# Kernel tuning notes

Measured on AMD Instinct MI355X. Metric: run time of the kernel, lower is better.

The kernel has to match this reference:

```python
import jax, jax.numpy as jnp
import numpy as np
import itertools


def _dwconv(x, w, b, pad, dil):
    # depthwise conv3d, x: [B,C,H,W,D], w: [C,1,k,k,k]
    out = jax.lax.conv_general_dilated(
        x, w, (1, 1, 1), [(pad, pad)] * 3, rhs_dilation=(dil, dil, dil),
        dimension_numbers=('NCDHW', 'OIDHW', 'NCDHW'), feature_group_count=x.shape[1])
    return out + b[None, :, None, None, None]


def _conv(x, w, b, pad):
    out = jax.lax.conv_general_dilated(
        x, w, (1, 1, 1), [(pad, pad)] * 3,
        dimension_numbers=('NCDHW', 'OIDHW', 'NCDHW'))
    return out + b[None, :, None, None, None]


def _pw(x, w, b):
    # 1x1x1 conv: x [B,C,H,W,D], w [O,C]
    return jnp.einsum('bchwd,oc->bohwd', x, w) + b[None, :, None, None, None]


def _deform_conv3d(x, off_w, off_b, w, b):
    # DeformConvPack-style: offsets from a regular 3x3x3 conv, then
    # trilinearly-interpolated gather at (base + kernel tap + offset), then GEMM.
    B, C, H, W, D = x.shape
    K = 27
    dt = x.dtype
    off = _conv(x, off_w, off_b, 1).reshape(B, K, 3, H, W, D)  # per-tap (dh,dw,dd)
    gh = jnp.arange(H, dtype=dt)
    gw = jnp.arange(W, dtype=dt)
    gd = jnp.arange(D, dtype=dt)
    base = jnp.stack(jnp.meshgrid(gh, gw, gd, indexing='ij'), 0)  # [3,H,W,D]
    t = jnp.arange(-1, 2, dtype=dt)  # kernel taps, padding=1
    taps = jnp.stack(jnp.meshgrid(t, t, t, indexing='ij'), -1).reshape(K, 3)
    pos = base[None] + taps[:, :, None, None, None]  # [K,3,H,W,D]
    pos = pos[None] + off  # [B,K,3,H,W,D]
    i0 = jnp.floor(pos)
    frac = pos - i0  # [B,K,3,H,W,D]
    i0 = i0.astype(jnp.int32)
    N = H * W * D
    xf = x.reshape(B, C, N)
    hi = jnp.array([H - 1, W - 1, D - 1], jnp.int32)[None, None, :, None, None, None]
    acc = jnp.zeros((B, C, K * N), dt)
    for corner in itertools.product((0, 1), repeat=3):
        c = jnp.array(corner, jnp.int32)[None, None, :, None, None, None]
        idx = i0 + c
        wgt = jnp.prod(jnp.where(c == 1, frac, 1.0 - frac), axis=2)  # [B,K,H,W,D]
        valid = jnp.all((idx >= 0) & (idx <= hi), axis=2)
        ic = jnp.clip(idx, 0, hi)
        flat = (ic[:, :, 0] * W + ic[:, :, 1]) * D + ic[:, :, 2]  # [B,K,H,W,D]
        g = jnp.take_along_axis(xf, flat.reshape(B, 1, K * N), axis=2)  # [B,C,K*N]
        acc = acc + g * (wgt * valid.astype(dt)).reshape(B, 1, K * N)
    sampled = acc.reshape(B, C, K, N)
    out = jnp.einsum('bckn,ock->bon', sampled, w.reshape(w.shape[0], C, K))
    out = out + b[None, :, None]
    return out.reshape(B, -1, H, W, D)


def _forward(x, proj1_w, proj1_b, conv0_w, conv0_b, convsp_w, convsp_b,
             off_w, off_b, dcn_w, dcn_b, conv1_w, conv1_b, proj2_w, proj2_b,
             B, C, H, W, D):
    xv = jnp.transpose(x, (0, 2, 1)).reshape(B, C, H, W, D)
    shortcut = xv
    h = jax.nn.gelu(_pw(xv, proj1_w, proj1_b), approximate=False)
    u = h
    a = _dwconv(h, conv0_w, conv0_b, 2, 1)        # 5x5x5 depthwise
    a = _dwconv(a, convsp_w, convsp_b, 9, 3)      # 7x7x7 depthwise, dilation 3
    a = _deform_conv3d(a, off_w, off_b, dcn_w, dcn_b)
    a = _pw(a, conv1_w, conv1_b)
    h = u * a
    h = _pw(h, proj2_w, proj2_b)
    out = h + shortcut
    return jnp.transpose(out.reshape(B, C, H * W * D), (0, 2, 1))


def setup_inputs() -> dict:
    key = jax.random.key(0)
    ks = jax.random.split(key, 8)
    B, C, H, W, D = 1, 64, 32, 32, 32
    N = H * W * D
    r = lambda k, s, sc: jax.random.normal(k, s, jnp.float32) * np.float32(sc)
    inv = lambda f: 1.0 / np.sqrt(f)
    return {
        'x': jax.random.normal(ks[0], (B, N, C), jnp.float32),
        'proj1_w': r(ks[1], (C, C), inv(C)), 'proj1_b': jnp.zeros((C,), jnp.float32),
        'conv0_w': r(ks[2], (C, 1, 5, 5, 5), inv(125)), 'conv0_b': jnp.zeros((C,), jnp.float32),
        'convsp_w': r(ks[3], (C, 1, 7, 7, 7), inv(343)), 'convsp_b': jnp.zeros((C,), jnp.float32),
        'off_w': r(ks[4], (81, C, 3, 3, 3), 0.01 * inv(27 * C)), 'off_b': jnp.zeros((81,), jnp.float32),
        'dcn_w': r(ks[5], (C, C, 3, 3, 3), inv(27 * C)), 'dcn_b': jnp.zeros((C,), jnp.float32),
        'conv1_w': r(ks[6], (C, C), inv(C)), 'conv1_b': jnp.zeros((C,), jnp.float32),
        'proj2_w': r(ks[7], (C, C), inv(C)), 'proj2_b': jnp.zeros((C,), jnp.float32),
        'B': B, 'C': C, 'H': H, 'W': W, 'D': D,
    }


def reference(x, proj1_w, proj1_b, conv0_w, conv0_b, convsp_w, convsp_b,
              off_w, off_b, dcn_w, dcn_b, conv1_w, conv1_b, proj2_w, proj2_b,
              B, C, H, W, D):
    return _forward(x, proj1_w, proj1_b, conv0_w, conv0_b, convsp_w, convsp_b,
                    off_w, off_b, dcn_w, dcn_b, conv1_w, conv1_b, proj2_w, proj2_b,
                    B, C, H, W, D)
```

## Files before the change

### kernel.cpp

```cpp
#include <hip/hip_runtime.h>
#include <math.h>

#define NSP 32768
#define NCH 64

typedef _Float16 half8 __attribute__((ext_vector_type(8)));
typedef _Float16 half4 __attribute__((ext_vector_type(4)));
typedef _Float16 half2v __attribute__((ext_vector_type(2)));
typedef float f32x4 __attribute__((ext_vector_type(4)));

__global__ __launch_bounds__(256) void k_proj1m(const float* __restrict__ x,
        const half8* __restrict__ Wp1, const float* __restrict__ b,
        _Float16* __restrict__ Uh) {
    __shared__ __align__(16) _Float16 Sx[64 * 72];
    int t = threadIdx.x;
    int n0 = blockIdx.x * 64;
    int lane = t & 63, wv = t >> 6;
    for (int i = wv; i < 64; i += 4) {
        float v = x[(size_t)(n0 + i) * 64 + lane];
        Sx[i * 72 + lane] = (_Float16)v;
    }
    __syncthreads();
    int pl = lane & 15, g = lane >> 4;
    int ob = wv;
    const half8* wbase = Wp1 + ob * 64 + lane;
    #pragma unroll
    for (int nt = 0; nt < 4; ++nt) {
        f32x4 acc4 = {0.f, 0.f, 0.f, 0.f};
        const _Float16* sb = &Sx[(nt * 16 + pl) * 72 + g * 8];
        #pragma unroll
        for (int kb = 0; kb < 2; ++kb) {
            half8 af = wbase[kb * 256];
            half8 bf = *(const half8*)(sb + kb * 32);
            acc4 = __builtin_amdgcn_mfma_f32_16x16x32_f16(af, bf, acc4, 0, 0, 0);
        }
        int n = n0 + nt * 16 + pl;
        #pragma unroll
        for (int r = 0; r < 4; ++r) {
            int o = ob * 16 + g * 4 + r;
            float a = acc4[r] + b[o];
            float gv = 0.5f * a * (1.0f + erff(a * 0.70710678118654752f));
            Uh[(size_t)o * NSP + n] = (_Float16)gv;
        }
    }
}

__global__ __launch_bounds__(256) void k_dw5(const _Float16* __restrict__ in,
        const float* __restrict__ w, const float* __restrict__ b,
        _Float16* __restrict__ out) {
    __shared__ float Sb5[2][20 * 38];
    int t = threadIdx.x;
    int bid = blockIdx.x;
    int blk = (bid & 7) * 128 + (bid >> 3);
    int c  = blk >> 4;
    int hq = (blk >> 1) & 7;
    int wq = blk & 1;
    int d  = t & 31;
    int wbloc = t >> 5;
    int wb = wq * 8 + wbloc;
    const float* wc = w + c * 125;
    const _Float16* src = in + ((size_t)c << 15);

    for (int idx = t; idx < 160; idx += 256) {
        int bi = idx / 80, r = idx % 80;
        int wi = r >> 2, e = r & 3;
        int Dp = (e < 2) ? e : 32 + e;
        Sb5[bi][wi * 38 + Dp] = 0.f;
    }

    float bc = b[c];
    float acc[4][2];
    #pragma unroll
    for (int a = 0; a < 4; ++a) { acc[a][0] = bc; acc[a][1] = bc; }

    #define STAGE5(m)                                                        \
        { int hh_ = 4 * hq + (m) - 2;                                        \
          if ((unsigned)hh_ < 32u) {                                         \
            const _Float16* row_ = src + (hh_ << 10);                        \
            for (int idx = t; idx < 80; idx += 256) {                        \
                int wi = idx >> 2, oct = idx & 3;                            \
                int wj = 16 * wq - 2 + wi;                                   \
                half8 vv = (half8)(_Float16)0.f;                             \
                if ((unsigned)wj < 32u)                                      \
                    vv = *(const half8*)&row_[(wj << 5) + oct * 8];          \
                float* dst = &Sb5[(m) & 1][wi * 38 + 2 + oct * 8];           \
                dst[0] = (float)vv[0]; dst[1] = (float)vv[1];                \
                dst[2] = (float)vv[2]; dst[3] = (float)vv[3];                \
                dst[4] = (float)vv[4]; dst[5] = (float)vv[5];                \
                dst[6] = (float)vv[6]; dst[7] = (float)vv[7];                \
            } } }

    STAGE5(0)
    __syncthreads();
    #pragma unroll 1
    for (int m = 0; m < 8; ++m) {
        if (m < 7) STAGE5(m + 1)
        int hh = 4 * hq + m - 2;
        if ((unsigned)hh < 32u) {
            float v[6][5];
            const float* sb = &Sb5[m & 1][0];
            #pragma unroll
            for (int jc = 0; jc < 6; ++jc)
                #pragma unroll
                for (int l = 0; l < 5; ++l)
                    v[jc][l] = sb[(2 * wbloc + jc) * 38 + d + l];
            #pragma unroll
            for (int a = 0; a < 4; ++a) {
                if (a <= m && m <= a + 4) {
                    const float* wr = wc + (m - a) * 25;
                    float s0 = 0.f, s1 = 0.f;
                    #pragma unroll
                    for (int j = 0; j < 5; ++j)
                        #pragma unroll
                        for (int l = 0; l < 5; ++l) {
                            float wv2 = wr[j * 5 + l];
                            s0 += wv2 * v[j][l];
                            s1 += wv2 * v[j + 1][l];
                        }
                    acc[a][0] += s0;
                    acc[a][1] += s1;
                }
            }
        }
        __syncthreads();
    }
    #pragma unroll
    for (int a = 0; a < 4; ++a)
        #pragma unroll
        for (int bb = 0; bb < 2; ++bb)
            out[(size_t)c * NSP + ((4 * hq + a) << 10) + ((2 * wb + bb) << 5) + d]
                = (_Float16)acc[a][bb];
    #undef STAGE5
}

__global__ __launch_bounds__(256) void k_dw7(const _Float16* __restrict__ in,
        const float* __restrict__ w, const float* __restrict__ b,
        _Float16* __restrict__ out) {
    __shared__ float Sb7[2][26 * 52];
    int t = threadIdx.x;
    int bid = blockIdx.x;
    int blk = (bid & 7) * 96 + (bid >> 3);
    int c  = blk / 12;
    int h0 = (blk % 12) >> 2;
    int wq = blk & 3;
    int d  = t & 31;
    int wloc = t >> 5;
    int w_ = wq * 8 + wloc;
    const float* wc = w + c * 343;
    const _Float16* src = in + ((size_t)c << 15);

    for (int idx = t; idx < 936; idx += 256) {
        int bi = idx / 468, r = idx % 468;
        int wi = r / 18, e = r % 18;
        int Dp = (e < 9) ? e : 32 + e;
        Sb7[bi][wi * 52 + Dp] = 0.f;
    }

    float bc = b[c];
    float acc[11];
    #pragma unroll
    for (int a = 0; a < 11; ++a) acc[a] = bc;

    #define STAGE7(m)                                                        \
        { int hh_ = h0 + 3 * (m) - 9;                                        \
          if ((unsigned)hh_ < 32u) {                                         \
            const _Float16* row_ = src + (hh_ << 10);                        \
            for (int idx = t; idx < 104; idx += 256) {                       \
                int wi = idx >> 2, oct = idx & 3;                            \
                int wj = 8 * wq - 9 + wi;                                    \
                half8 vv = (half8)(_Float16)0.f;                             \
                if ((unsigned)wj < 32u)                                      \
                    vv = *(const half8*)&row_[(wj << 5) + oct * 8];          \
                float* dst = &Sb7[(m) & 1][wi * 52 + 9 + oct * 8];           \
                dst[0] = (float)vv[0]; dst[1] = (float)vv[1];                \
                dst[2] = (float)vv[2]; dst[3] = (float)vv[3];                \
                dst[4] = (float)vv[4]; dst[5] = (float)vv[5];                \
                dst[6] = (float)vv[6]; dst[7] = (float)vv[7];                \
            } } }

    STAGE7(0)
    __syncthreads();
    #pragma unroll 1
    for (int m = 0; m < 17; ++m) {
        if (m < 16) STAGE7(m + 1)
        int hh = h0 + 3 * m - 9;
        if ((unsigned)hh < 32u) {
            float vf[49];
            const float* sb = &Sb7[m & 1][0];
            #pragma unroll
            for (int jw = 0; jw < 7; ++jw)
                #pragma unroll
                for (int l = 0; l < 7; ++l)
                    vf[jw * 7 + l] = sb[(wloc + 3 * jw) * 52 + d + 3 * l];
            #pragma unroll
            for (int a = 0; a < 11; ++a) {
                if (a <= m && m <= a + 6) {
                    const float* wr = wc + (m - a) * 49;
                    float sA = 0.f, sB = 0.f;
                    #pragma unroll
                    for (int q = 0; q < 24; ++q) {
                        sA = fmaf(wr[2 * q],     vf[2 * q],     sA);
                        sB = fmaf(wr[2 * q + 1], vf[2 * q + 1], sB);
                    }
                    acc[a] += sA + sB + wr[48] * vf[48];
                }
            }
        }
        __syncthreads();
    }
    #pragma unroll
    for (int a = 0; a < 11; ++a) {
        int h = h0 + 3 * a;
        if (h < 32)
            out[(size_t)c * NSP + (h << 10) + (w_ << 5) + d] = (_Float16)acc[a];
    }
    #undef STAGE7
}

__global__ __launch_bounds__(256) void k_tr(const _Float16* __restrict__ in,
        _Float16* __restrict__ outh) {
    __shared__ __align__(16) _Float16 tile[64 * 74];
    int t = threadIdx.x;
    int n0 = blockIdx.x * 64;
    #pragma unroll
    for (int i = 0; i < 2; ++i) {
        int u = i * 256 + t;
        int c = u >> 3, oct = u & 7;
        half8 v = *(const half8*)&in[(size_t)c * NSP + n0 + oct * 8];
        *(half8*)&tile[c * 74 + oct * 8] = v;
    }
    __syncthreads();
    #pragma unroll
    for (int i = 0; i < 2; ++i) {
        int u = i * 256 + t;
        int nl = u >> 3, co = u & 7;
        half8 r;
        #pragma unroll
        for (int j = 0; j < 8; ++j) r[j] = tile[(co * 8 + j) * 74 + nl];
        *(half8*)&outh[(size_t)(n0 + nl) * 64 + co * 8] = r;
    }
}

__global__ __launch_bounds__(256) void k_wpack(const float* __restrict__ dw,
        _Float16* __restrict__ Wp) {
    int idx = blockIdx.x * 256 + threadIdx.x;
    int j = idx & 7;
    int l = (idx >> 3) & 63;
    int obk = idx >> 9;
    int ob = obk & 3, kb = obk >> 2;
    int o = ob * 16 + (l & 15);
    int Kp = kb * 32 + (l >> 4) * 8 + j;
    int k = Kp >> 6, c = Kp & 63;
    Wp[idx] = (_Float16)dw[(size_t)o * 1728 + c * 27 + k];
}

__global__ __launch_bounds__(256) void k_wpack_off(const float* __restrict__ ow,
        _Float16* __restrict__ Wp2) {
    int idx = blockIdx.x * 256 + threadIdx.x;
    int j = idx & 7;
    int l = (idx >> 3) & 63;
    int obk = idx >> 9;
    int ob = obk % 6, kb = obk / 6;
    int o = ob * 16 + (l & 15);
    int Kp = kb * 32 + (l >> 4) * 8 + j;
    int k = Kp >> 6, c = Kp & 63;
    Wp2[idx] = (o < 81) ? (_Float16)ow[(size_t)o * 1728 + c * 27 + k]
                        : (_Float16)0.f;
}

__global__ __launch_bounds__(256) void k_wpack64(const float* __restrict__ w,
        _Float16* __restrict__ Wp) {
    int idx = blockIdx.x * 256 + threadIdx.x;
    int j = idx & 7;
    int l = (idx >> 3) & 63;
    int obk = idx >> 9;
    int ob = obk & 3, kb = obk >> 2;
    int o = ob * 16 + (l & 15);
    int Kp = kb * 32 + (l >> 4) * 8 + j;
    Wp[idx] = (_Float16)w[o * 64 + Kp];
}

__global__ __launch_bounds__(384) void k_offg(const _Float16* __restrict__ aTh,
        const half8* __restrict__ Wp2, const float* __restrict__ obias,
        float* __restrict__ off) {
    __shared__ __align__(16) _Float16 S2[2][4 * 34 * 72];
    int t = threadIdx.x;
    int bid = blockIdx.x;
    int blk = (bid & 7) * 64 + (bid >> 3);
    int h = blk >> 4, w0 = (blk & 15) * 2;
    int n0 = (h << 10) + (w0 << 5);
    int lane = t & 63, wv = t >> 6;
    int co8 = (lane & 7) << 3;

    for (int u = t; u < 1152; u += 384) {
        int bi = u / 576, r2 = u % 576;
        int nbw = r2 / 144, r3 = r2 % 144;
        int dd = (r3 >= 72) ? 33 : 0, cc = r3 % 72;
        S2[bi][(nbw * 34 + dd) * 72 + cc] = (_Float16)0.f;
    }

    int pl = lane & 15, g = lane >> 4;
    int obi = wv;
    f32x4 acc[4];
    #pragma unroll
    for (int i = 0; i < 4; ++i) acc[i] = (f32x4){0.f, 0.f, 0.f, 0.f};
    const half8* wb = Wp2 + obi * 64 + lane;

    #define OSTAGE(kh)                                                        \
        { int hh_ = h + (kh) - 1;                                            \
          bool okh_ = (unsigned)hh_ < 32u;                                   \
          for (int u = wv; u < 16; u += 6) {                                 \
              int nbw = u >> 2, oct = u & 3;                                 \
              int wj = w0 + nbw - 1;                                         \
              int di = oct * 8 + (lane >> 3);                                \
              bool ok = okh_ & ((unsigned)wj < 32u);                         \
              half8 vv = (half8)(_Float16)0.f;                               \
              if (ok) vv = *(const half8*)(aTh +                             \
                  ((size_t)((((hh_ << 5) + wj) << 5) + di)) * 64 + co8);     \
              *(half8*)&S2[(kh) & 1][(nbw * 34 + 1 + di) * 72 + co8] = vv;   \
          } }

    #define OCOMP(kh)                                                        \
        { const _Float16* sb = &S2[(kh) & 1][pl * 72 + g * 8];               \
          _Pragma("unroll")                                                  \
          for (int kk = 0; kk < 18; ++kk) {                                  \
              int kglob = (kh) * 9 + (kk >> 1);                              \
              int kw3 = (kglob / 3) % 3, kd = kglob % 3;                     \
              half8 af = wb[(size_t)((kh) * 18 + kk) * 384];                 \
              _Pragma("unroll")                                              \
              for (int pt = 0; pt < 4; ++pt) {                               \
                  int row = ((pt >> 1) + kw3) * 34 + (pt & 1) * 16 + kd;     \
                  half8 bf = *(const half8*)(sb + row * 72 + (kk & 1) * 32); \
                  acc[pt] = __builtin_amdgcn_mfma_f32_16x16x32_f16(          \
                                af, bf, acc[pt], 0, 0, 0);                   \
              }                                                              \
          } }

    OSTAGE(0)
    __syncthreads();
    OSTAGE(1)
    OCOMP(0)
    __syncthreads();
    OSTAGE(2)
    OCOMP(1)
    __syncthreads();
    OCOMP(2)
    #undef OSTAGE
    #undef OCOMP

    #pragma unroll
    for (int pt = 0; pt < 4; ++pt) {
        #pragma unroll
        for (int r = 0; r < 4; ++r) {
            int o = obi * 16 + g * 4 + r;
            if (o < 81)
                off[(size_t)o * NSP + n0 + pt * 16 + pl] = acc[pt][r] + obias[o];
        }
    }
}

__global__ __launch_bounds__(256) void k_deform(const _Float16* __restrict__ aTh,
        const float* __restrict__ off, const half8* __restrict__ Wp,
        const float* __restrict__ db, _Float16* __restrict__ dcnT) {
    __shared__ __align__(16) _Float16 S[32 * 456];
    __shared__ __align__(16) _Float16 TPF[864 * 4];
    __shared__ int TPv[864];
    int t = threadIdx.x;
    int bid = blockIdx.x;
    int blk = (bid & 7) * 128 + (bid >> 3);
    int n0 = blk * 32;
    int lane = t & 63, wv = t >> 6;

    for (int idx = t; idx < 864; idx += 256) {
        int p = idx & 31, k = idx >> 5;
        int n = n0 + p;
        int h = n >> 10, w = (n >> 5) & 31, d = n & 31;
        float ph = (float)(h + k / 9 - 1)       + off[(size_t)(k * 3 + 0) * NSP + n];
        float pw = (float)(w + (k / 3) % 3 - 1) + off[(size_t)(k * 3 + 1) * NSP + n];
        float pd = (float)(d + k % 3 - 1)       + off[(size_t)(k * 3 + 2) * NSP + n];
        float fh = floorf(ph), fw = floorf(pw), fd = floorf(pd);
        int ih = (int)fh, iw = (int)fw, id = (int)fd;
        int nb0 = ih * 1024 + iw * 32 + id;
        int mask = 0;
        #pragma unroll
        for (int cb = 0; cb < 8; ++cb) {
            int hh = ih + ((cb >> 2) & 1);
            int wq = iw + ((cb >> 1) & 1);
            int dq = id + (cb & 1);
            bool ok = ((unsigned)hh < 32u) & ((unsigned)wq < 32u) & ((unsigned)dq < 32u);
            mask |= (ok ? 1 : 0) << cb;
        }
        TPv[idx] = ((nb0 + 4096) << 8) | mask;
        half4 f;
        f[0] = (_Float16)(ph - fh);
        f[1] = (_Float16)(pw - fw);
        f[2] = (_Float16)(pd - fd);
        f[3] = (_Float16)0.f;
        *(half4*)&TPF[idx * 4] = f;
    }
    __syncthreads();

    int p8 = lane >> 3, co = lane & 7;
    int pl = lane & 15, g = lane >> 4;
    f32x4 acc[2];
    acc[0] = (f32x4){0.f, 0.f, 0.f, 0.f};
    acc[1] = (f32x4){0.f, 0.f, 0.f, 0.f};
    const half8* wbase = Wp + wv * 64 + lane;
    const _Float16* sbase0 = &S[pl * 456 + g * 8];
    const _Float16* sbase1 = &S[(16 + pl) * 456 + g * 8];

    #define DCHUNK(T0, NT)                                                   \
        for (int u = wv; u < (NT) * 4; u += 4) {                             \
            int kk = u >> 2, pg = u & 3;                                     \
            int p = pg * 8 + p8;                                             \
            int tap = ((T0) + kk) * 32 + p;                                  \
            int v = TPv[tap];                                                \
            int nb = (v >> 8) - 4096, mask = v & 255;                        \
            half4 f = *(const half4*)&TPF[tap * 4];                          \
            _Float16 one = (_Float16)1.f;                                    \
            _Float16 rh = f[0], rw = f[1], rd = f[2];                        \
            _Float16 h0 = one - rh, w0 = one - rw, d0 = one - rd;            \
            _Float16 t00 = h0 * w0, t01 = h0 * rw;                           \
            _Float16 t10 = rh * w0, t11 = rh * rw;                           \
            half2v a0 = (half2v)0, a1 = (half2v)0, a2 = (half2v)0,           \
                   a3 = (half2v)0;                                           \
            _Pragma("unroll")                                                \
            for (int i = 0; i < 8; ++i) {                                    \
                int nn = nb + ((i >> 2) & 1) * 1024 + ((i >> 1) & 1) * 32    \
                       + (i & 1);                                            \
                bool okc = (mask >> i) & 1;                                  \
                size_t ad = okc ? ((size_t)nn << 6) : 0;                     \
                half8 vv = *(const half8*)(aTh + ad + (co << 3));            \
                _Float16 txy = (i & 4) ? ((i & 2) ? t11 : t10)               \
                                       : ((i & 2) ? t01 : t00);              \
                _Float16 wg = txy * ((i & 1) ? rd : d0);                     \
                wg = okc ? wg : (_Float16)0.f;                               \
                half2v wg2 = {wg, wg};                                       \
                a0 += (half2v){vv[0], vv[1]} * wg2;                          \
                a1 += (half2v){vv[2], vv[3]} * wg2;                          \
                a2 += (half2v){vv[4], vv[5]} * wg2;                          \
                a3 += (half2v){vv[6], vv[7]} * wg2;                          \
            }                                                                \
            half8 r;                                                         \
            r[0] = a0[0]; r[1] = a0[1]; r[2] = a1[0]; r[3] = a1[1];          \
            r[4] = a2[0]; r[5] = a2[1]; r[6] = a3[0]; r[7] = a3[1];          \
            *(half8*)&S[p * 456 + kk * 64 + (co << 3)] = r;                  \
        }                                                                    \
        __syncthreads();                                                     \
        _Pragma("unroll")                                                    \
        for (int kb = 0; kb < (NT) * 2; ++kb) {                              \
            half8 af = wbase[(size_t)(2 * (T0) + kb) * 256];                 \
            half8 bf0 = *(const half8*)(sbase0 + kb * 32);                   \
            half8 bf1 = *(const half8*)(sbase1 + kb * 32);                   \
            acc[0] = __builtin_amdgcn_mfma_f32_16x16x32_f16(af, bf0,         \
                         acc[0], 0, 0, 0);                                   \
            acc[1] = __builtin_amdgcn_mfma_f32_16x16x32_f16(af, bf1,         \
                         acc[1], 0, 0, 0);                                   \
        }                                                                    \
        __syncthreads();

    DCHUNK(0, 7)
    DCHUNK(7, 7)
    DCHUNK(14, 7)
    DCHUNK(21, 6)
    #undef DCHUNK

    #pragma unroll
    for (int pt = 0; pt < 2; ++pt) {
        half4 hv;
        #pragma unroll
        for (int r2 = 0; r2 < 4; ++r2) {
            int o = wv * 16 + g * 4 + r2;
            hv[r2] = (_Float16)(acc[pt][r2] + db[o]);
        }
        *(half4*)&dcnT[(size_t)(n0 + pt * 16 + pl) * 64 + wv * 16 + g * 4] = hv;
    }
}

__global__ __launch_bounds__(256) void k_finalm(const _Float16* __restrict__ dcnT,
        const _Float16* __restrict__ Uh, const float* __restrict__ x,
        const half8* __restrict__ Wc1, const float* __restrict__ c1b,
        const half8* __restrict__ Wp2f, const float* __restrict__ p2b,
        float* __restrict__ out) {
    __shared__ __align__(16) _Float16 Sd[64 * 72];
    __shared__ __align__(16) _Float16 Sh[64 * 72];
    int t = threadIdx.x;
    int n0 = blockIdx.x * 64;
    int lane = t & 63, wv = t >> 6;
    #pragma unroll
    for (int i = 0; i < 2; ++i) {
        int u = i * 256 + t;
        int nl = u >> 3, oct = u & 7;
        *(half8*)&Sd[nl * 72 + oct * 8] =
            *(const half8*)&dcnT[(size_t)(n0 + nl) * 64 + oct * 8];
    }
    __syncthreads();

    int pl = lane & 15, g = lane >> 4;
    int ob = wv;
    const half8* w1 = Wc1 + ob * 64 + lane;
    #pragma unroll
    for (int nt = 0; nt < 4; ++nt) {
        f32x4 acc4 = {0.f, 0.f, 0.f, 0.f};
        const _Float16* sb = &Sd[(nt * 16 + pl) * 72 + g * 8];
        #pragma unroll
        for (int kb = 0; kb < 2; ++kb) {
            half8 af = w1[kb * 256];
            half8 bf = *(const half8*)(sb + kb * 32);
            acc4 = __builtin_amdgcn_mfma_f32_16x16x32_f16(af, bf, acc4, 0, 0, 0);
        }
        int n = n0 + nt * 16 + pl;
        int o0 = ob * 16 + g * 4;
        float4 bb = *(const float4*)&c1b[o0];
        half4 hv;
        hv[0] = (_Float16)((float)Uh[(size_t)(o0 + 0) * NSP + n] * (acc4[0] + bb.x));
        hv[1] = (_Float16)((float)Uh[(size_t)(o0 + 1) * NSP + n] * (acc4[1] + bb.y));
        hv[2] = (_Float16)((float)Uh[(size_t)(o0 + 2) * NSP + n] * (acc4[2] + bb.z));
        hv[3] = (_Float16)((float)Uh[(size_t)(o0 + 3) * NSP + n] * (acc4[3] + bb.w));
        *(half4*)&Sh[(nt * 16 + pl) * 72 + o0] = hv;
    }
    __syncthreads();

    const half8* w2 = Wp2f + ob * 64 + lane;
    #pragma unroll
    for (int nt = 0; nt < 4; ++nt) {
        f32x4 acc4 = {0.f, 0.f, 0.f, 0.f};
        const _Float16* sb = &Sh[(nt * 16 + pl) * 72 + g * 8];
        #pragma unroll
        for (int kb = 0; kb < 2; ++kb) {
            half8 af = w2[kb * 256];
            half8 bf = *(const half8*)(sb + kb * 32);
            acc4 = __builtin_amdgcn_mfma_f32_16x16x32_f16(af, bf, acc4, 0, 0, 0);
        }
        int n = n0 + nt * 16 + pl;
        int o0 = ob * 16 + g * 4;
        float4 bb = *(const float4*)&p2b[o0];
        float4 xr = *(const float4*)&x[(size_t)n * 64 + o0];
        float4 ov;
        ov.x = acc4[0] + bb.x + xr.x;
        ov.y = acc4[1] + bb.y + xr.y;
        ov.z = acc4[2] + bb.z + xr.z;
        ov.w = acc4[3] + bb.w + xr.w;
        *(float4*)&out[(size_t)n * 64 + o0] = ov;
    }
}

extern "C" void kernel_launch(void* const* d_in, const int* in_sizes, int n_in,
                              void* d_out, int out_size, void* d_ws, size_t ws_size,
                              hipStream_t stream) {
    const float* x   = (const float*)d_in[0];
    const float* p1w = (const float*)d_in[1];
    const float* p1b = (const float*)d_in[2];
    const float* c0w = (const float*)d_in[3];
    const float* c0b = (const float*)d_in[4];
    const float* csw = (const float*)d_in[5];
    const float* csb = (const float*)d_in[6];
    const float* ofw = (const float*)d_in[7];
    const float* ofb = (const float*)d_in[8];
    const float* dcw = (const float*)d_in[9];
    const float* dcb = (const float*)d_in[10];
    const float* c1w = (const float*)d_in[11];
    const float* c1b = (const float*)d_in[12];
    const float* p2w = (const float*)d_in[13];
    const float* p2b = (const float*)d_in[14];
    float* out = (float*)d_out;

    char* ws = (char*)d_ws;
    const size_t CN2 = (size_t)NCH * NSP * 2;
    _Float16* Uh   = (_Float16*)(ws);
    _Float16* T0h  = (_Float16*)(ws + CN2);
    _Float16* T1h  = (_Float16*)(ws + 2 * CN2);
    _Float16* aTh  = (_Float16*)(ws + 3 * CN2);
    float*    OFFp = (float*)(ws + 4 * CN2);
    _Float16* dcnT = (_Float16*)(ws + 4 * CN2 + (size_t)81 * NSP * 4);
    _Float16* Wp   = dcnT + (size_t)NSP * 64;
    _Float16* Wp2  = Wp + 110592;
    _Float16* Wp1  = Wp2 + 165888;
    _Float16* Wc1  = Wp1 + 4096;
    _Float16* Wp2f = Wc1 + 4096;

    k_wpack64  <<<16, 256, 0, stream>>>(p1w, Wp1);
    k_wpack64  <<<16, 256, 0, stream>>>(c1w, Wc1);
    k_wpack64  <<<16, 256, 0, stream>>>(p2w, Wp2f);
    k_wpack    <<<432, 256, 0, stream>>>(dcw, Wp);
    k_wpack_off<<<648, 256, 0, stream>>>(ofw, Wp2);
    k_proj1m   <<<NSP / 64, 256, 0, stream>>>(x, (const half8*)Wp1, p1b, Uh);
    k_dw5      <<<1024, 256, 0, stream>>>(Uh, c0w, c0b, T0h);
    k_dw7      <<<768, 256, 0, stream>>>(T0h, csw, csb, T1h);
    k_tr       <<<NSP / 64, 256, 0, stream>>>(T1h, aTh);
    k_offg     <<<512, 384, 0, stream>>>(aTh, (const half8*)Wp2, ofb, OFFp);
    k_deform   <<<1024, 256, 0, stream>>>(aTh, OFFp, (const half8*)Wp, dcb, dcnT);
    k_finalm   <<<NSP / 64, 256, 0, stream>>>(dcnT, Uh, x, (const half8*)Wc1, c1b,
                                              (const half8*)Wp2f, p2b, out);
}
```

Before: 125.5 us.

## Store offsets point-major, halve offg tile, merge weight-pack kernels

The offset conv output moves from channel-major [81][N] to point-major [N][27x4], with each tap padded to a float4. This lets the deform kernel fetch each tap's (dh,dw,dd) with one vector load instead of three strided loads. The offset GEMM kernel now handles one w-column (32 points) per block with twice as many blocks, and transposes results through LDS for coalesced float4 stores. The five weight-packing launches are merged into one kernel. The costs are a larger offset buffer (108 vs 81 floats per point), an extra LDS pass with syncs, and less weight reuse per offg block.

Measured after the change: 120.8 us. 3.7% less time.

```diff
diff --git a/kernel.cpp b/kernel.cpp
--- a/kernel.cpp
+++ b/kernel.cpp
@@ -241,95 +241,104 @@
     }
 }
 
-__global__ __launch_bounds__(256) void k_wpack(const float* __restrict__ dw,
-        _Float16* __restrict__ Wp) {
-    int idx = blockIdx.x * 256 + threadIdx.x;
-    int j = idx & 7;
-    int l = (idx >> 3) & 63;
-    int obk = idx >> 9;
-    int ob = obk & 3, kb = obk >> 2;
-    int o = ob * 16 + (l & 15);
-    int Kp = kb * 32 + (l >> 4) * 8 + j;
-    int k = Kp >> 6, c = Kp & 63;
-    Wp[idx] = (_Float16)dw[(size_t)o * 1728 + c * 27 + k];
-}
-
-__global__ __launch_bounds__(256) void k_wpack_off(const float* __restrict__ ow,
+__global__ __launch_bounds__(256) void k_wpack_all(
+        const float* __restrict__ p1w, const float* __restrict__ c1w,
+        const float* __restrict__ p2w, const float* __restrict__ dcw,
+        const float* __restrict__ ofw,
+        _Float16* __restrict__ Wp1, _Float16* __restrict__ Wc1,
+        _Float16* __restrict__ Wp2f, _Float16* __restrict__ Wp,
         _Float16* __restrict__ Wp2) {
-    int idx = blockIdx.x * 256 + threadIdx.x;
-    int j = idx & 7;
-    int l = (idx >> 3) & 63;
-    int obk = idx >> 9;
-    int ob = obk % 6, kb = obk / 6;
-    int o = ob * 16 + (l & 15);
-    int Kp = kb * 32 + (l >> 4) * 8 + j;
-    int k = Kp >> 6, c = Kp & 63;
-    Wp2[idx] = (o < 81) ? (_Float16)ow[(size_t)o * 1728 + c * 27 + k]
-                        : (_Float16)0.f;
-}
-
-__global__ __launch_bounds__(256) void k_wpack64(const float* __restrict__ w,
-        _Float16* __restrict__ Wp) {
-    int idx = blockIdx.x * 256 + threadIdx.x;
-    int j = idx & 7;
-    int l = (idx >> 3) & 63;
-    int obk = idx >> 9;
-    int ob = obk & 3, kb = obk >> 2;
-    int o = ob * 16 + (l & 15);
-    int Kp = kb * 32 + (l >> 4) * 8 + j;
-    Wp[idx] = (_Float16)w[o * 64 + Kp];
+    int bidx = blockIdx.x;
+    int t = threadIdx.x;
+    if (bidx < 48) {
+        const float* w = (bidx < 16) ? p1w : (bidx < 32) ? c1w : p2w;
+        _Float16* Wd   = (bidx < 16) ? Wp1 : (bidx < 32) ? Wc1 : Wp2f;
+        int idx = (bidx & 15) * 256 + t;
+        int j = idx & 7;
+        int l = (idx >> 3) & 63;
+        int obk = idx >> 9;
+        int ob = obk & 3, kb = obk >> 2;
+        int o = ob * 16 + (l & 15);
+        int Kp = kb * 32 + (l >> 4) * 8 + j;
+        Wd[idx] = (_Float16)w[o * 64 + Kp];
+    } else if (bidx < 480) {
+        int idx = (bidx - 48) * 256 + t;
+        int j = idx & 7;
+        int l = (idx >> 3) & 63;
+        int obk = idx >> 9;
+        int ob = obk & 3, kb = obk >> 2;
+        int o = ob * 16 + (l & 15);
+        int Kp = kb * 32 + (l >> 4) * 8 + j;
+        int k = Kp >> 6, c = Kp & 63;
+        Wp[idx] = (_Float16)dcw[(size_t)o * 1728 + c * 27 + k];
+    } else {
+        int idx = (bidx - 480) * 256 + t;
+        int j = idx & 7;
+        int l = (idx >> 3) & 63;
+        int obk = idx >> 9;
+        int ob = obk % 6, kb = obk / 6;
+        int o = ob * 16 + (l & 15);
+        int Kp = kb * 32 + (l >> 4) * 8 + j;
+        int k = Kp >> 6, c = Kp & 63;
+        Wp2[idx] = (o < 81) ? (_Float16)ofw[(size_t)o * 1728 + c * 27 + k]
+                            : (_Float16)0.f;
+    }
 }
 
 __global__ __launch_bounds__(384) void k_offg(const _Float16* __restrict__ aTh,
         const half8* __restrict__ Wp2, const float* __restrict__ obias,
-        float* __restrict__ off) {
-    __shared__ __align__(16) _Float16 S2[2][4 * 34 * 72];
+        float* __restrict__ OFFn) {
+    __shared__ __align__(16) char SMEM[29376];
+    _Float16* S2 = (_Float16*)SMEM;
+    float*    TF = (float*)SMEM;
+    const int SB = 3 * 34 * 72;
     int t = threadIdx.x;
     int bid = blockIdx.x;
-    int blk = (bid & 7) * 64 + (bid >> 3);
-    int h = blk >> 4, w0 = (blk & 15) * 2;
-    int n0 = (h << 10) + (w0 << 5);
+    int blk = (bid & 7) * 128 + (bid >> 3);
+    int h = blk >> 5, w = blk & 31;
+    int n0 = blk << 5;
     int lane = t & 63, wv = t >> 6;
     int co8 = (lane & 7) << 3;
 
-    for (int u = t; u < 1152; u += 384) {
-        int bi = u / 576, r2 = u % 576;
+    for (int u = t; u < 864; u += 384) {
+        int bi = u / 432, r2 = u % 432;
         int nbw = r2 / 144, r3 = r2 % 144;
         int dd = (r3 >= 72) ? 33 : 0, cc = r3 % 72;
-        S2[bi][(nbw * 34 + dd) * 72 + cc] = (_Float16)0.f;
+        S2[bi * SB + (nbw * 34 + dd) * 72 + cc] = (_Float16)0.f;
     }
 
     int pl = lane & 15, g = lane >> 4;
     int obi = wv;
-    f32x4 acc[4];
-    #pragma unroll
-    for (int i = 0; i < 4; ++i) acc[i] = (f32x4){0.f, 0.f, 0.f, 0.f};
+    f32x4 acc[2];
+    acc[0] = (f32x4){0.f, 0.f, 0.f, 0.f};
+    acc[1] = (f32x4){0.f, 0.f, 0.f, 0.f};
     const half8* wb = Wp2 + obi * 64 + lane;
 
     #define OSTAGE(kh)                                                        \
         { int hh_ = h + (kh) - 1;                                            \
           bool okh_ = (unsigned)hh_ < 32u;                                   \
-          for (int u = wv; u < 16; u += 6) {                                 \
+          for (int u = wv; u < 12; u += 6) {                                 \
               int nbw = u >> 2, oct = u & 3;                                 \
-              int wj = w0 + nbw - 1;                                         \
+              int wj = w + nbw - 1;                                          \
               int di = oct * 8 + (lane >> 3);                                \
               bool ok = okh_ & ((unsigned)wj < 32u);                         \
               half8 vv = (half8)(_Float16)0.f;                               \
               if (ok) vv = *(const half8*)(aTh +                             \
                   ((size_t)((((hh_ << 5) + wj) << 5) + di)) * 64 + co8);     \
-              *(half8*)&S2[(kh) & 1][(nbw * 34 + 1 + di) * 72 + co8] = vv;   \
+              *(half8*)&S2[((kh) & 1) * SB + (nbw * 34 + 1 + di) * 72 + co8] \
+                  = vv;                                                      \
           } }
 
     #define OCOMP(kh)                                                        \
-        { const _Float16* sb = &S2[(kh) & 1][pl * 72 + g * 8];               \
+        { const _Float16* sb = &S2[((kh) & 1) * SB + pl * 72 + g * 8];       \
           _Pragma("unroll")                                                  \
           for (int kk = 0; kk < 18; ++kk) {                                  \
               int kglob = (kh) * 9 + (kk >> 1);                              \
               int kw3 = (kglob / 3) % 3, kd = kglob % 3;                     \
               half8 af = wb[(size_t)((kh) * 18 + kk) * 384];                 \
               _Pragma("unroll")                                              \
-              for (int pt = 0; pt < 4; ++pt) {                               \
-                  int row = ((pt >> 1) + kw3) * 34 + (pt & 1) * 16 + kd;     \
+              for (int pt = 0; pt < 2; ++pt) {                               \
+                  int row = kw3 * 34 + pt * 16 + kd;                         \
                   half8 bf = *(const half8*)(sb + row * 72 + (kk & 1) * 32); \
                   acc[pt] = __builtin_amdgcn_mfma_f32_16x16x32_f16(          \
                                 af, bf, acc[pt], 0, 0, 0);                   \
@@ -348,19 +357,29 @@
     #undef OSTAGE
     #undef OCOMP
 
-    #pragma unroll
-    for (int pt = 0; pt < 4; ++pt) {
+    __syncthreads();
+    #pragma unroll
+    for (int pt = 0; pt < 2; ++pt) {
+        int pos = pt * 16 + pl;
         #pragma unroll
         for (int r = 0; r < 4; ++r) {
             int o = obi * 16 + g * 4 + r;
-            if (o < 81)
-                off[(size_t)o * NSP + n0 + pt * 16 + pl] = acc[pt][r] + obias[o];
-        }
+            if (o < 81) {
+                int slot = (o / 3) * 4 + o % 3;
+                TF[pos * 108 + slot] = acc[pt][r] + obias[o];
+            }
+        }
+    }
+    __syncthreads();
+    for (int u = t; u < 864; u += 384) {
+        int row = u / 27, q = u - row * 27;
+        float4 v = *(const float4*)&TF[row * 108 + q * 4];
+        *(float4*)&OFFn[(size_t)(n0 + row) * 108 + q * 4] = v;
     }
 }
 
 __global__ __launch_bounds__(256) void k_deform(const _Float16* __restrict__ aTh,
-        const float* __restrict__ off, const half8* __restrict__ Wp,
+        const float* __restrict__ OFFn, const half8* __restrict__ Wp,
         const float* __restrict__ db, _Float16* __restrict__ dcnT) {
     __shared__ __align__(16) _Float16 S[32 * 456];
     __shared__ __align__(16) _Float16 TPF[864 * 4];
@@ -375,9 +394,10 @@
         int p = idx & 31, k = idx >> 5;
         int n = n0 + p;
         int h = n >> 10, w = (n >> 5) & 31, d = n & 31;
-        float ph = (float)(h + k / 9 - 1)       + off[(size_t)(k * 3 + 0) * NSP + n];
-        float pw = (float)(w + (k / 3) % 3 - 1) + off[(size_t)(k * 3 + 1) * NSP + n];
-        float pd = (float)(d + k % 3 - 1)       + off[(size_t)(k * 3 + 2) * NSP + n];
+        float4 ov = *(const float4*)&OFFn[(size_t)n * 108 + k * 4];
+        float ph = (float)(h + k / 9 - 1)       + ov.x;
+        float pw = (float)(w + (k / 3) % 3 - 1) + ov.y;
+        float pd = (float)(d + k % 3 - 1)       + ov.z;
         float fh = floorf(ph), fw = floorf(pw), fd = floorf(pd);
         int ih = (int)fh, iw = (int)fw, id = (int)fd;
         int nb0 = ih * 1024 + iw * 32 + id;
@@ -571,25 +591,22 @@
     _Float16* T0h  = (_Float16*)(ws + CN2);
     _Float16* T1h  = (_Float16*)(ws + 2 * CN2);
     _Float16* aTh  = (_Float16*)(ws + 3 * CN2);
-    float*    OFFp = (float*)(ws + 4 * CN2);
-    _Float16* dcnT = (_Float16*)(ws + 4 * CN2 + (size_t)81 * NSP * 4);
+    float*    OFFn = (float*)(ws + 4 * CN2);
+    _Float16* dcnT = (_Float16*)(ws + 4 * CN2 + (size_t)NSP * 108 * 4);
     _Float16* Wp   = dcnT + (size_t)NSP * 64;
     _Float16* Wp2  = Wp + 110592;
     _Float16* Wp1  = Wp2 + 165888;
     _Float16* Wc1  = Wp1 + 4096;
     _Float16* Wp2f = Wc1 + 4096;
 
-    k_wpack64  <<<16, 256, 0, stream>>>(p1w, Wp1);
-    k_wpack64  <<<16, 256, 0, stream>>>(c1w, Wc1);
-    k_wpack64  <<<16, 256, 0, stream>>>(p2w, Wp2f);
-    k_wpack    <<<432, 256, 0, stream>>>(dcw, Wp);
-    k_wpack_off<<<648, 256, 0, stream>>>(ofw, Wp2);
+    k_wpack_all<<<1128, 256, 0, stream>>>(p1w, c1w, p2w, dcw, ofw,
+                                          Wp1, Wc1, Wp2f, Wp, Wp2);
     k_proj1m   <<<NSP / 64, 256, 0, stream>>>(x, (const half8*)Wp1, p1b, Uh);
     k_dw5      <<<1024, 256, 0, stream>>>(Uh, c0w, c0b, T0h);
     k_dw7      <<<768, 256, 0, stream>>>(T0h, csw, csb, T1h);
     k_tr       <<<NSP / 64, 256, 0, stream>>>(T1h, aTh);
-    k_offg     <<<512, 384, 0, stream>>>(aTh, (const half8*)Wp2, ofb, OFFp);
-    k_deform   <<<1024, 256, 0, stream>>>(aTh, OFFp, (const half8*)Wp, dcb, dcnT);
+    k_offg     <<<1024, 384, 0, stream>>>(aTh, (const half8*)Wp2, ofb, OFFn);
+    k_deform   <<<1024, 256, 0, stream>>>(aTh, OFFn, (const half8*)Wp, dcb, dcnT);
     k_finalm   <<<NSP / 64, 256, 0, stream>>>(dcnT, Uh, x, (const half8*)Wc1, c1b,
                                               (const half8*)Wp2f, p2b, out);
 }
```
